# Kernel optimization log

Hardware: AMD Instinct MI355X
Metric: run time of the kernel (lower is better)

## Reference

```python
import jax, jax.numpy as jnp
import numpy as np

BS = 128      # outer batch (was bs=8 in original)
NR = 3        # num_ref
C_DATA = 64
C_GT = 3
C_HID = 256
H = W = 32


def setup_inputs() -> dict:
    key = jax.random.key(0)
    k1, k2, k3, k4 = jax.random.split(key, 4)
    data = jax.random.normal(k1, (BS * NR, C_DATA, H, W), dtype=jnp.float32)
    gt = jax.random.normal(k2, (BS, C_GT, H, W), dtype=jnp.float32)
    # 1x1 conv weights == per-pixel dense layers
    W1 = jax.random.normal(k3, (C_HID, C_DATA + C_GT), dtype=jnp.float32) * 0.05
    b1 = jnp.zeros((C_HID,), dtype=jnp.float32)
    W3 = jax.random.normal(k4, (1, C_HID), dtype=jnp.float32) * 0.05
    b3 = jnp.zeros((1,), dtype=jnp.float32)
    return {"data": data, "gt": gt, "W1": W1, "b1": b1, "W3": W3, "b3": b3}


def reference(data, gt, W1, b1, W3, b3):
    # data: [BS*NR, 64, H, W] -> [BS, NR, 64, H, W]
    d = data.reshape(BS, NR, C_DATA, H, W)
    # gt[i] repeated over NR refs -> broadcast instead of looping over batch
    g = jnp.broadcast_to(gt[:, None], (BS, NR, C_GT, H, W))
    x = jnp.concatenate([d, g], axis=2)                      # [BS, NR, 67, H, W]
    # 1x1 conv -> relu  (feature_1)
    f1 = jax.nn.relu(jnp.einsum('bnchw,oc->bnohw', x, W1)
                     + b1[None, None, :, None, None])        # [BS, NR, 256, H, W]
    # 1x1 conv -> sigmoid (feature_3, feature_4)
    s = jax.nn.sigmoid(jnp.einsum('bnchw,oc->bnohw', f1, W3)
                       + b3[None, None, :, None, None])      # [BS, NR, 1, H, W]
    # normalize weights over the num_ref dim (torch dim=0 within each batch item)
    w = s / jnp.sum(s, axis=1, keepdims=True)                # [BS, NR, 1, H, W]
    # weighted sum over refs; w broadcasts over the 64 channels
    z = jnp.sum(d * w, axis=1)                               # [BS, 64, H, W]
    return z, w
```

## Files before the change

### kernel.cpp

```cpp
#include <hip/hip_runtime.h>
#include <hip/hip_bf16.h>

#define BS 128
#define NR 3
#define CD 64
#define CG 3
#define CH 256
#define HW 1024
#define K_IN 67
#define NKB 12
#define P 64

typedef __attribute__((ext_vector_type(8))) short bf16x8;
typedef __attribute__((ext_vector_type(4))) float f32x4;

static __device__ __forceinline__ short f2bf(float x) {
    union { __hip_bfloat16 b; short s; } c;
    c.b = __float2bfloat16(x);
    return c.s;
}
static __device__ __forceinline__ float bf2f(short s) {
    union { unsigned u; float f; } c;
    c.u = (unsigned)(unsigned short)s << 16;
    return c.f;
}

__global__ __launch_bounds__(256) void prep_kernel(
    const float* __restrict__ W1, const float* __restrict__ b1,
    short* __restrict__ w1f)
{
    const int fid  = blockIdx.x * 256 + threadIdx.x;
    const int mt   = fid / 192;
    const int rem  = fid % 192;
    const int t    = rem >> 6;
    const int lane = rem & 63;
    const int row  = mt * 16 + (lane & 15);
    const int k0   = t * 32 + (lane >> 4) * 8;
    bf16x8 v;
#pragma unroll
    for (int j = 0; j < 8; ++j) {
        const int k = k0 + j;
        float val = 0.f;
        if (k < K_IN)       val = W1[row * K_IN + k];
        else if (k == K_IN) val = b1[row];
        v[j] = f2bf(val);
    }
    *(bf16x8*)&w1f[(size_t)fid * 8] = v;
}

__global__ __launch_bounds__(256) void fused_kernel(
    const float* __restrict__ data, const float* __restrict__ gt,
    const short* __restrict__ w1f, const float* __restrict__ W3,
    const float* __restrict__ b3, float* __restrict__ out)
{
    __shared__ short xls[NR * NKB * P * 8];
    __shared__ float p_lds[4][NR * P];
    __shared__ float s_lds[NR][P];
    __shared__ float w_lds[NR][P];

    const int tid  = threadIdx.x;
    const int lane = tid & 63;
    const int wave = tid >> 6;
    const int b    = blockIdx.x >> 4;
    const int pt0  = (blockIdx.x & 15) * P;

    {
        const int px = tid & 63;
        const int gp = pt0 + px;
#pragma unroll
        for (int i = 0; i < 9; ++i) {
            const int it  = wave * 9 + i;
            const int ref = it / NKB, kb = it % NKB;
            bf16x8 v;
#pragma unroll
            for (int j = 0; j < 8; ++j) {
                const int k = kb * 8 + j;
                float val = 0.f;
                if (k < CD)         val = data[((size_t)(b * NR + ref) * CD + k) * HW + gp];
                else if (k < K_IN)  val = gt[((size_t)b * CG + (k - CD)) * HW + gp];
                else if (k == K_IN) val = 1.0f;
                v[j] = f2bf(val);
            }
            *(bf16x8*)&xls[((ref * NKB + kb) * P + px) * 8] = v;
        }
    }

    const int col = lane & 15, kq = lane >> 4;
    bf16x8 afrag[4][3];
#pragma unroll
    for (int i = 0; i < 4; ++i)
#pragma unroll
        for (int t = 0; t < 3; ++t)
            afrag[i][t] = *(const bf16x8*)&w1f[(((size_t)(wave * 4 + i) * 3 + t) * 64 + lane) * 8];
    float w3v[4][4];
#pragma unroll
    for (int i = 0; i < 4; ++i)
#pragma unroll
        for (int r = 0; r < 4; ++r)
            w3v[i][r] = W3[wave * 64 + i * 16 + kq * 4 + r];

    __syncthreads();

#pragma unroll
    for (int nt = 0; nt < NR * 4; ++nt) {
        const int ref = nt >> 2, pn0 = (nt & 3) * 16;
        bf16x8 bfrag[3];
#pragma unroll
        for (int t = 0; t < 3; ++t)
            bfrag[t] = *(const bf16x8*)&xls[((ref * NKB + t * 4 + kq) * P + pn0 + col) * 8];

        f32x4 acc[4];
#pragma unroll
        for (int i = 0; i < 4; ++i) acc[i] = (f32x4){0.f, 0.f, 0.f, 0.f};
#pragma unroll
        for (int t = 0; t < 3; ++t)
#pragma unroll
            for (int i = 0; i < 4; ++i)
                acc[i] = __builtin_amdgcn_mfma_f32_16x16x32_bf16(
                    afrag[i][t], bfrag[t], acc[i], 0, 0, 0);

        float partial = 0.f;
#pragma unroll
        for (int i = 0; i < 4; ++i)
#pragma unroll
            for (int r = 0; r < 4; ++r)
                partial += w3v[i][r] * fmaxf(acc[i][r], 0.f);
        partial += __shfl_xor(partial, 16);
        partial += __shfl_xor(partial, 32);
        if (lane < 16) p_lds[wave][ref * P + pn0 + lane] = partial;
    }
    __syncthreads();

    if (tid < NR * P) {
        const float t = p_lds[0][tid] + p_lds[1][tid] + p_lds[2][tid]
                      + p_lds[3][tid] + b3[0];
        s_lds[tid >> 6][tid & 63] = 1.f / (1.f + __expf(-t));
    }
    __syncthreads();

    float* wout = out + (size_t)BS * CD * HW;
    if (tid < P) {
        const float s0 = s_lds[0][tid], s1 = s_lds[1][tid], s2 = s_lds[2][tid];
        const float inv = 1.f / (s0 + s1 + s2);
        const float w0 = s0 * inv, w1 = s1 * inv, w2 = s2 * inv;
        w_lds[0][tid] = w0; w_lds[1][tid] = w1; w_lds[2][tid] = w2;
        wout[((size_t)b * NR + 0) * HW + pt0 + tid] = w0;
        wout[((size_t)b * NR + 1) * HW + pt0 + tid] = w1;
        wout[((size_t)b * NR + 2) * HW + pt0 + tid] = w2;
    }
    __syncthreads();

    {
        const int px = tid & 63, grp = tid >> 6;
        const float w0 = w_lds[0][px], w1 = w_lds[1][px], w2 = w_lds[2][px];
        const int gp = pt0 + px;
#pragma unroll
        for (int q = 0; q < 2; ++q) {
            const int kb = grp * 2 + q;
            const bf16x8 v0 = *(const bf16x8*)&xls[((0 * NKB + kb) * P + px) * 8];
            const bf16x8 v1 = *(const bf16x8*)&xls[((1 * NKB + kb) * P + px) * 8];
            const bf16x8 v2 = *(const bf16x8*)&xls[((2 * NKB + kb) * P + px) * 8];
#pragma unroll
            for (int j = 0; j < 8; ++j) {
                const float z = w0 * bf2f(v0[j]) + w1 * bf2f(v1[j]) + w2 * bf2f(v2[j]);
                out[((size_t)b * CD + kb * 8 + j) * HW + gp] = z;
            }
        }
    }
}

extern "C" void kernel_launch(void* const* d_in, const int* in_sizes, int n_in,
                              void* d_out, int out_size, void* d_ws, size_t ws_size,
                              hipStream_t stream)
{
    const float* data = (const float*)d_in[0];
    const float* gt   = (const float*)d_in[1];
    const float* W1   = (const float*)d_in[2];
    const float* b1   = (const float*)d_in[3];
    const float* W3   = (const float*)d_in[4];
    const float* b3   = (const float*)d_in[5];
    float* out  = (float*)d_out;
    short* w1f  = (short*)d_ws;

    prep_kernel<<<12, 256, 0, stream>>>(W1, b1, w1f);
    fused_kernel<<<BS * (HW / P), 256, 0, stream>>>(data, gt, w1f, W3, b3, out);
}
```

Measured before the change: 216.4 us.

## Vectorize global loads/stores with float4 and repack LDS into 4-channel groups

Replaces the scalar per-pixel global loads of data with float4 loads issued in two batches of six, and stores them into a new LDS layout of 4-channel groups per pixel. The gt channels and bias column go into a separate small padded LDS tile. B fragments are assembled from two 4-wide LDS reads. The final weighted-sum output is written as float4. Also adds an occupancy hint of 4 blocks per CU. The aim is to cut global memory transaction count and improve load coalescing. In exchange the kernel does more scalar LDS stores, which risks bank conflicts.

New measurement: 174.3 us. 19.5% less time.

```diff
diff --git a/kernel.cpp b/kernel.cpp
--- a/kernel.cpp
+++ b/kernel.cpp
@@ -8,9 +8,9 @@
 #define CH 256
 #define HW 1024
 #define K_IN 67
-#define NKB 12
 #define P 64
 
+typedef __attribute__((ext_vector_type(4))) short bf16x4;
 typedef __attribute__((ext_vector_type(8))) short bf16x8;
 typedef __attribute__((ext_vector_type(4))) float f32x4;
 
@@ -48,12 +48,14 @@
     *(bf16x8*)&w1f[(size_t)fid * 8] = v;
 }
 
-__global__ __launch_bounds__(256) void fused_kernel(
+__global__ __launch_bounds__(256, 4) void fused_kernel(
     const float* __restrict__ data, const float* __restrict__ gt,
     const short* __restrict__ w1f, const float* __restrict__ W3,
     const float* __restrict__ b3, float* __restrict__ out)
 {
-    __shared__ short xls[NR * NKB * P * 8];
+    __shared__ short xls[NR * 16 * P * 4];
+    __shared__ short gtp[P * 4];
+    __shared__ short zp[P * 4];
     __shared__ float p_lds[4][NR * P];
     __shared__ float s_lds[NR][P];
     __shared__ float w_lds[NR][P];
@@ -63,29 +65,8 @@
     const int wave = tid >> 6;
     const int b    = blockIdx.x >> 4;
     const int pt0  = (blockIdx.x & 15) * P;
-
-    {
-        const int px = tid & 63;
-        const int gp = pt0 + px;
-#pragma unroll
-        for (int i = 0; i < 9; ++i) {
-            const int it  = wave * 9 + i;
-            const int ref = it / NKB, kb = it % NKB;
-            bf16x8 v;
-#pragma unroll
-            for (int j = 0; j < 8; ++j) {
-                const int k = kb * 8 + j;
-                float val = 0.f;
-                if (k < CD)         val = data[((size_t)(b * NR + ref) * CD + k) * HW + gp];
-                else if (k < K_IN)  val = gt[((size_t)b * CG + (k - CD)) * HW + gp];
-                else if (k == K_IN) val = 1.0f;
-                v[j] = f2bf(val);
-            }
-            *(bf16x8*)&xls[((ref * NKB + kb) * P + px) * 8] = v;
-        }
-    }
-
-    const int col = lane & 15, kq = lane >> 4;
+    const int col  = lane & 15, kq = lane >> 4;
+
     bf16x8 afrag[4][3];
 #pragma unroll
     for (int i = 0; i < 4; ++i)
@@ -99,6 +80,34 @@
         for (int r = 0; r < 4; ++r)
             w3v[i][r] = W3[wave * 64 + i * 16 + kq * 4 + r];
 
+    if (tid < P) *(bf16x4*)&zp[tid * 4] = (bf16x4){0, 0, 0, 0};
+    {
+        const int c = tid >> 6, px = tid & 63;
+        if (c < CG) gtp[px * 4 + c] = f2bf(gt[((size_t)b * CG + c) * HW + pt0 + px]);
+        else        gtp[px * 4 + 3] = (short)0x3F80;
+    }
+
+#pragma unroll
+    for (int half = 0; half < 2; ++half) {
+        float4 ld[6];
+#pragma unroll
+        for (int u = 0; u < 6; ++u) {
+            const int q = (half * 6 + u) * 256 + tid;
+            const int ref = q >> 10, ch = (q >> 4) & 63, p4 = q & 15;
+            ld[u] = *(const float4*)(data + ((size_t)(b * NR + ref) * CD + ch) * HW + pt0 + 4 * p4);
+        }
+#pragma unroll
+        for (int u = 0; u < 6; ++u) {
+            const int q = (half * 6 + u) * 256 + tid;
+            const int ref = q >> 10, ch = (q >> 4) & 63, p4 = q & 15;
+            short* xp = &xls[((ref * 16 + (ch >> 2)) * P + 4 * p4) * 4 + (ch & 3)];
+            xp[0]  = f2bf(ld[u].x);
+            xp[4]  = f2bf(ld[u].y);
+            xp[8]  = f2bf(ld[u].z);
+            xp[12] = f2bf(ld[u].w);
+        }
+    }
+
     __syncthreads();
 
 #pragma unroll
@@ -106,8 +115,21 @@
         const int ref = nt >> 2, pn0 = (nt & 3) * 16;
         bf16x8 bfrag[3];
 #pragma unroll
-        for (int t = 0; t < 3; ++t)
-            bfrag[t] = *(const bf16x8*)&xls[((ref * NKB + t * 4 + kq) * P + pn0 + col) * 8];
+        for (int t = 0; t < 3; ++t) {
+            const short* plo;
+            const short* phi;
+            if (t < 2) {
+                const int c2 = t * 8 + kq * 2;
+                plo = &xls[((ref * 16 + c2)     * P) * 4];
+                phi = &xls[((ref * 16 + c2 + 1) * P) * 4];
+            } else {
+                plo = (kq == 0) ? gtp : zp;
+                phi = zp;
+            }
+            const bf16x4 lo = *(const bf16x4*)&plo[(pn0 + col) * 4];
+            const bf16x4 hi = *(const bf16x4*)&phi[(pn0 + col) * 4];
+            bfrag[t] = __builtin_shufflevector(lo, hi, 0, 1, 2, 3, 4, 5, 6, 7);
+        }
 
         f32x4 acc[4];
 #pragma unroll
@@ -150,22 +172,22 @@
     }
     __syncthreads();
 
-    {
-        const int px = tid & 63, grp = tid >> 6;
-        const float w0 = w_lds[0][px], w1 = w_lds[1][px], w2 = w_lds[2][px];
-        const int gp = pt0 + px;
-#pragma unroll
-        for (int q = 0; q < 2; ++q) {
-            const int kb = grp * 2 + q;
-            const bf16x8 v0 = *(const bf16x8*)&xls[((0 * NKB + kb) * P + px) * 8];
-            const bf16x8 v1 = *(const bf16x8*)&xls[((1 * NKB + kb) * P + px) * 8];
-            const bf16x8 v2 = *(const bf16x8*)&xls[((2 * NKB + kb) * P + px) * 8];
-#pragma unroll
-            for (int j = 0; j < 8; ++j) {
-                const float z = w0 * bf2f(v0[j]) + w1 * bf2f(v1[j]) + w2 * bf2f(v2[j]);
-                out[((size_t)b * CD + kb * 8 + j) * HW + gp] = z;
-            }
-        }
+#pragma unroll
+    for (int u = 0; u < 4; ++u) {
+        const int q = u * 256 + tid;
+        const int ch = q >> 4, p4 = q & 15;
+        float zx = 0.f, zy = 0.f, zz = 0.f, zw = 0.f;
+#pragma unroll
+        for (int ref = 0; ref < NR; ++ref) {
+            const float4 wv = *(const float4*)&w_lds[ref][4 * p4];
+            const short* xp = &xls[((ref * 16 + (ch >> 2)) * P + 4 * p4) * 4 + (ch & 3)];
+            zx += wv.x * bf2f(xp[0]);
+            zy += wv.y * bf2f(xp[4]);
+            zz += wv.z * bf2f(xp[8]);
+            zw += wv.w * bf2f(xp[12]);
+        }
+        const float4 zv = {zx, zy, zz, zw};
+        *(float4*)(out + ((size_t)b * CD + ch) * HW + pt0 + 4 * p4) = zv;
     }
 }
 
```
